# Kernel tuning notes

Hardware: AMD Instinct MI355X
Metric: run time of the kernel (lower is better)

The kernel has to match this reference:

```python
import jax, jax.numpy as jnp
import numpy as np

N = 2097152  # batch of 3x3 matrices


def setup_inputs() -> dict:
    key = jax.random.key(0)
    k1, k2 = jax.random.split(key)
    rotation = jax.random.normal(k1, (N, 3, 3), dtype=jnp.float32)
    # learned parameter: eye(3) + 1e-3 * randn, per __init__
    mat = jnp.eye(3, dtype=jnp.float32) + 0.001 * jax.random.normal(k2, (3, 3), dtype=jnp.float32)
    return {"rotation": rotation, "mat": mat}


def reference(rotation, mat):
    # new_mat = mat @ rotation (mat broadcast over batch)  -> [N,3,3]
    new_mat = jnp.einsum('ab,nbc->nac', mat, rotation)
    # polar rotation factor via batched 3x3 SVD: R = U @ V^T
    U, S, Vh = jnp.linalg.svd(new_mat, full_matrices=False)
    out = jnp.einsum('nab,nbc->nac', U, Vh)  # torch: U @ V.transpose == U @ Vh
    logdet = jnp.zeros((rotation.shape[0],), dtype=rotation.dtype)
    return out, logdet
```

## Files before the change

kernel.cpp:

```cpp
#include <hip/hip_runtime.h>
#include <math.h>


typedef float v2f __attribute__((ext_vector_type(2)));
typedef float v4f __attribute__((ext_vector_type(4)));

#define NEWTON_ITERS 6
#define NS_ITERS 2

__device__ __forceinline__ void polar_pair(
    v2f& x00, v2f& x01, v2f& x02,
    v2f& x10, v2f& x11, v2f& x12,
    v2f& x20, v2f& x21, v2f& x22)
{
    #pragma unroll
    for (int it = 0; it < NEWTON_ITERS; ++it) {
        v2f c00 = x11*x22 - x12*x21;
        v2f c01 = x12*x20 - x10*x22;
        v2f c02 = x10*x21 - x11*x20;
        v2f c10 = x02*x21 - x01*x22;
        v2f c11 = x00*x22 - x02*x20;
        v2f c12 = x01*x20 - x00*x21;
        v2f c20 = x01*x12 - x02*x11;
        v2f c21 = x02*x10 - x00*x12;
        v2f c22 = x00*x11 - x01*x10;

        v2f det = x00*c00 + x01*c01 + x02*c02;

        float d0 = det.x, d1 = det.y;
        float ad0 = fmaxf(fabsf(d0), 1e-30f);
        float ad1 = fmaxf(fabsf(d1), 1e-30f);
        float z0 = __builtin_amdgcn_exp2f(__builtin_amdgcn_logf(ad0) * (-1.0f/3.0f));
        float z1 = __builtin_amdgcn_exp2f(__builtin_amdgcn_logf(ad1) * (-1.0f/3.0f));
        v2f s = {0.5f * z0, 0.5f * z1};
        v2f u = {copysignf(0.5f * z0 * z0, d0), copysignf(0.5f * z1 * z1, d1)};

        x00 = s*x00 + u*c00;  x01 = s*x01 + u*c01;  x02 = s*x02 + u*c02;
        x10 = s*x10 + u*c10;  x11 = s*x11 + u*c11;  x12 = s*x12 + u*c12;
        x20 = s*x20 + u*c20;  x21 = s*x21 + u*c21;  x22 = s*x22 + u*c22;
    }

    #pragma unroll
    for (int it = 0; it < NS_ITERS; ++it) {
        v2f s00 = x00*x00 + x10*x10 + x20*x20;
        v2f s01 = x00*x01 + x10*x11 + x20*x21;
        v2f s02 = x00*x02 + x10*x12 + x20*x22;
        v2f s11 = x01*x01 + x11*x11 + x21*x21;
        v2f s12 = x01*x02 + x11*x12 + x21*x22;
        v2f s22 = x02*x02 + x12*x12 + x22*x22;
        v2f t00 = 1.5f - 0.5f*s00, t01 = -0.5f*s01, t02 = -0.5f*s02;
        v2f t11 = 1.5f - 0.5f*s11, t12 = -0.5f*s12;
        v2f t22 = 1.5f - 0.5f*s22;
        v2f y00 = x00*t00 + x01*t01 + x02*t02;
        v2f y01 = x00*t01 + x01*t11 + x02*t12;
        v2f y02 = x00*t02 + x01*t12 + x02*t22;
        v2f y10 = x10*t00 + x11*t01 + x12*t02;
        v2f y11 = x10*t01 + x11*t11 + x12*t12;
        v2f y12 = x10*t02 + x11*t12 + x12*t22;
        v2f y20 = x20*t00 + x21*t01 + x22*t02;
        v2f y21 = x20*t01 + x21*t11 + x22*t12;
        v2f y22 = x20*t02 + x21*t12 + x22*t22;
        x00=y00; x01=y01; x02=y02;
        x10=y10; x11=y11; x12=y12;
        x20=y20; x21=y21; x22=y22;
    }
}

__device__ __forceinline__ void compute_tile(
    float* buf, int lane, float* outBase,
    float m00, float m01, float m02,
    float m10, float m11, float m12,
    float m20, float m21, float m22)
{
    const float* L = buf + lane * 18;
    v2f r00 = {L[0], L[9]},  r01 = {L[1], L[10]}, r02 = {L[2], L[11]};
    v2f r10 = {L[3], L[12]}, r11 = {L[4], L[13]}, r12 = {L[5], L[14]};
    v2f r20 = {L[6], L[15]}, r21 = {L[7], L[16]}, r22 = {L[8], L[17]};

    v2f x00 = m00*r00 + m01*r10 + m02*r20;
    v2f x01 = m00*r01 + m01*r11 + m02*r21;
    v2f x02 = m00*r02 + m01*r12 + m02*r22;
    v2f x10 = m10*r00 + m11*r10 + m12*r20;
    v2f x11 = m10*r01 + m11*r11 + m12*r21;
    v2f x12 = m10*r02 + m11*r12 + m12*r22;
    v2f x20 = m20*r00 + m21*r10 + m22*r20;
    v2f x21 = m20*r01 + m21*r11 + m22*r21;
    v2f x22 = m20*r02 + m21*r12 + m22*r22;

    polar_pair(x00,x01,x02,x10,x11,x12,x20,x21,x22);

    float* S = buf + lane * 18;
    S[0]=x00.x; S[9] =x00.y; S[1]=x01.x; S[10]=x01.y; S[2]=x02.x; S[11]=x02.y;
    S[3]=x10.x; S[12]=x10.y; S[4]=x11.x; S[13]=x11.y; S[5]=x12.x; S[14]=x12.y;
    S[6]=x20.x; S[15]=x20.y; S[7]=x21.x; S[16]=x21.y; S[8]=x22.x; S[17]=x22.y;

    v4f* g4 = (v4f*)outBase;
    const v4f* l4 = (const v4f*)buf;
    #pragma unroll
    for (int k = 0; k < 4; ++k)
        g4[k * 64 + lane] = l4[k * 64 + lane];
    ((v2f*)(outBase + 1024))[lane] = ((const v2f*)(buf + 1024))[lane];
}

__device__ __forceinline__ void stage_tile(const float* gsrc, float* buf, int lane)
{
    #pragma unroll
    for (int k = 0; k < 4; ++k) {
        __builtin_amdgcn_global_load_lds(
            (const __attribute__((address_space(1))) void*)(gsrc + k * 256 + lane * 4),
            (__attribute__((address_space(3))) void*)(buf + k * 256),
            16, 0, 0);
    }
    #pragma unroll
    for (int k = 0; k < 2; ++k) {
        __builtin_amdgcn_global_load_lds(
            (const __attribute__((address_space(1))) void*)(gsrc + 1024 + k * 64 + lane),
            (__attribute__((address_space(3))) void*)(buf + 1024 + k * 64),
            4, 0, 0);
    }
}

__global__ __launch_bounds__(256) void polar3x3_pipe_kernel(
    const float* __restrict__ rot,
    const float* __restrict__ mat,
    float* __restrict__ out,
    int n)
{
    __shared__ __align__(16) float lds[9216];
    const int t    = threadIdx.x;
    const int lane = t & 63;
    const int w    = t >> 6;
    const long long blockBase = (long long)blockIdx.x * 1024;
    const long long waveBase  = blockBase + (long long)w * 256;
    float* buf0 = lds + w * 2304;
    float* buf1 = buf0 + 1152;

    const float m00 = mat[0], m01 = mat[1], m02 = mat[2];
    const float m10 = mat[3], m11 = mat[4], m12 = mat[5];
    const float m20 = mat[6], m21 = mat[7], m22 = mat[8];

    const bool full = (blockBase + 1024 <= (long long)n);

    if (full) {
        stage_tile(rot + waveBase * 9, buf0, lane);
        stage_tile(rot + (waveBase + 128) * 9, buf1, lane);

        asm volatile("s_waitcnt vmcnt(6)" ::: "memory");

        v4f* ld4 = (v4f*)(out + (long long)n * 9 + waveBase);
        __builtin_nontemporal_store(v4f{0.f, 0.f, 0.f, 0.f}, ld4 + lane);

        compute_tile(buf0, lane, out + waveBase * 9,
                     m00,m01,m02,m10,m11,m12,m20,m21,m22);

        asm volatile("s_waitcnt vmcnt(6)" ::: "memory");

        compute_tile(buf1, lane, out + (waveBase + 128) * 9,
                     m00,m01,m02,m10,m11,m12,m20,m21,m22);
    } else {
        #pragma unroll
        for (int tile = 0; tile < 2; ++tile) {
            long long tileBase = waveBase + tile * 128;
            v2f r00,r01,r02,r10,r11,r12,r20,r21,r22;
            #pragma unroll
            for (int q = 0; q < 2; ++q) {
                long long mi = tileBase + 2 * lane + q;
                if (mi < (long long)n) {
                    const float* r = rot + mi * 9;
                    r00[q]=r[0]; r01[q]=r[1]; r02[q]=r[2];
                    r10[q]=r[3]; r11[q]=r[4]; r12[q]=r[5];
                    r20[q]=r[6]; r21[q]=r[7]; r22[q]=r[8];
                } else {
                    r00[q]=1.f; r01[q]=0.f; r02[q]=0.f;
                    r10[q]=0.f; r11[q]=1.f; r12[q]=0.f;
                    r20[q]=0.f; r21[q]=0.f; r22[q]=1.f;
                }
            }
            v2f x00 = m00*r00 + m01*r10 + m02*r20;
            v2f x01 = m00*r01 + m01*r11 + m02*r21;
            v2f x02 = m00*r02 + m01*r12 + m02*r22;
            v2f x10 = m10*r00 + m11*r10 + m12*r20;
            v2f x11 = m10*r01 + m11*r11 + m12*r21;
            v2f x12 = m10*r02 + m11*r12 + m12*r22;
            v2f x20 = m20*r00 + m21*r10 + m22*r20;
            v2f x21 = m20*r01 + m21*r11 + m22*r21;
            v2f x22 = m20*r02 + m21*r12 + m22*r22;
            polar_pair(x00,x01,x02,x10,x11,x12,x20,x21,x22);
            #pragma unroll
            for (int q = 0; q < 2; ++q) {
                long long mi = tileBase + 2 * lane + q;
                if (mi < (long long)n) {
                    float* o = out + mi * 9;
                    o[0]=x00[q]; o[1]=x01[q]; o[2]=x02[q];
                    o[3]=x10[q]; o[4]=x11[q]; o[5]=x12[q];
                    o[6]=x20[q]; o[7]=x21[q]; o[8]=x22[q];
                    out[(long long)n * 9 + mi] = 0.0f;
                }
            }
        }
    }
}

extern "C" void kernel_launch(void* const* d_in, const int* in_sizes, int n_in,
                              void* d_out, int out_size, void* d_ws, size_t ws_size,
                              hipStream_t stream) {
    const float* rot = (const float*)d_in[0];
    const float* mat = (const float*)d_in[1];
    float* out = (float*)d_out;

    int n = in_sizes[0] / 9;
    int block = 256;
    int grid = (n + 1023) / 1024;
    polar3x3_pipe_kernel<<<grid, block, 0, stream>>>(rot, mat, out, n);
}
```

Measured before the change: 30.61 us.

## Double each wave's work with four-tile LDS ping-pong pipeline and nontemporal stores

Each wave now handles 512 matrices as four 128-matrix tiles instead of two. After a tile is computed and stored, the next tile is staged into the freed LDS buffer, so global loads overlap with compute and vmcnt waits are retuned to match. Output stores become nontemporal, and the logdet zero stores are issued up front. The grid halves, which lowers wave count and occupancy-based latency hiding, and the vmcnt counts must exactly match the outstanding store and load ordering.

```diff
diff --git a/kernel.cpp b/kernel.cpp
--- a/kernel.cpp
+++ b/kernel.cpp
@@ -66,7 +66,25 @@
     }
 }
 
-__device__ __forceinline__ void compute_tile(
+__device__ __forceinline__ void stage_tile(const float* gsrc, float* buf, int lane)
+{
+    #pragma unroll
+    for (int k = 0; k < 4; ++k) {
+        __builtin_amdgcn_global_load_lds(
+            (const __attribute__((address_space(1))) void*)(gsrc + k * 256 + lane * 4),
+            (__attribute__((address_space(3))) void*)(buf + k * 256),
+            16, 0, 0);
+    }
+    #pragma unroll
+    for (int k = 0; k < 2; ++k) {
+        __builtin_amdgcn_global_load_lds(
+            (const __attribute__((address_space(1))) void*)(gsrc + 1024 + k * 64 + lane),
+            (__attribute__((address_space(3))) void*)(buf + 1024 + k * 64),
+            4, 0, 0);
+    }
+}
+
+__device__ __forceinline__ void compute_store_tile(
     float* buf, int lane, float* outBase,
     float m00, float m01, float m02,
     float m10, float m11, float m12,
@@ -98,29 +116,12 @@
     const v4f* l4 = (const v4f*)buf;
     #pragma unroll
     for (int k = 0; k < 4; ++k)
-        g4[k * 64 + lane] = l4[k * 64 + lane];
-    ((v2f*)(outBase + 1024))[lane] = ((const v2f*)(buf + 1024))[lane];
-}
-
-__device__ __forceinline__ void stage_tile(const float* gsrc, float* buf, int lane)
-{
-    #pragma unroll
-    for (int k = 0; k < 4; ++k) {
-        __builtin_amdgcn_global_load_lds(
-            (const __attribute__((address_space(1))) void*)(gsrc + k * 256 + lane * 4),
-            (__attribute__((address_space(3))) void*)(buf + k * 256),
-            16, 0, 0);
-    }
-    #pragma unroll
-    for (int k = 0; k < 2; ++k) {
-        __builtin_amdgcn_global_load_lds(
-            (const __attribute__((address_space(1))) void*)(gsrc + 1024 + k * 64 + lane),
-            (__attribute__((address_space(3))) void*)(buf + 1024 + k * 64),
-            4, 0, 0);
-    }
-}
-
-__global__ __launch_bounds__(256) void polar3x3_pipe_kernel(
+        __builtin_nontemporal_store(l4[k * 64 + lane], g4 + k * 64 + lane);
+    __builtin_nontemporal_store(((const v2f*)(buf + 1024))[lane],
+                                (v2f*)(outBase + 1024) + lane);
+}
+
+__global__ __launch_bounds__(256) void polar3x3_ss_kernel(
     const float* __restrict__ rot,
     const float* __restrict__ mat,
     float* __restrict__ out,
@@ -130,8 +131,8 @@
     const int t    = threadIdx.x;
     const int lane = t & 63;
     const int w    = t >> 6;
-    const long long blockBase = (long long)blockIdx.x * 1024;
-    const long long waveBase  = blockBase + (long long)w * 256;
+    const long long blockBase = (long long)blockIdx.x * 2048;
+    const long long waveBase  = blockBase + (long long)w * 512;
     float* buf0 = lds + w * 2304;
     float* buf1 = buf0 + 1152;
 
@@ -139,28 +140,37 @@
     const float m10 = mat[3], m11 = mat[4], m12 = mat[5];
     const float m20 = mat[6], m21 = mat[7], m22 = mat[8];
 
-    const bool full = (blockBase + 1024 <= (long long)n);
+    const bool full = (blockBase + 2048 <= (long long)n);
 
     if (full) {
-        stage_tile(rot + waveBase * 9, buf0, lane);
-        stage_tile(rot + (waveBase + 128) * 9, buf1, lane);
+        v4f* ld4 = (v4f*)(out + (long long)n * 9 + waveBase);
+        __builtin_nontemporal_store(v4f{0.f,0.f,0.f,0.f}, ld4 + lane);
+        __builtin_nontemporal_store(v4f{0.f,0.f,0.f,0.f}, ld4 + 64 + lane);
+
+        stage_tile(rot + waveBase * 9,           buf0, lane);
+        stage_tile(rot + (waveBase + 128) * 9,   buf1, lane);
 
         asm volatile("s_waitcnt vmcnt(6)" ::: "memory");
-
-        v4f* ld4 = (v4f*)(out + (long long)n * 9 + waveBase);
-        __builtin_nontemporal_store(v4f{0.f, 0.f, 0.f, 0.f}, ld4 + lane);
-
-        compute_tile(buf0, lane, out + waveBase * 9,
-                     m00,m01,m02,m10,m11,m12,m20,m21,m22);
-
-        asm volatile("s_waitcnt vmcnt(6)" ::: "memory");
-
-        compute_tile(buf1, lane, out + (waveBase + 128) * 9,
-                     m00,m01,m02,m10,m11,m12,m20,m21,m22);
+        compute_store_tile(buf0, lane, out + waveBase * 9,
+                           m00,m01,m02,m10,m11,m12,m20,m21,m22);
+        stage_tile(rot + (waveBase + 256) * 9, buf0, lane);
+
+        asm volatile("s_waitcnt vmcnt(11)" ::: "memory");
+        compute_store_tile(buf1, lane, out + (waveBase + 128) * 9,
+                           m00,m01,m02,m10,m11,m12,m20,m21,m22);
+        stage_tile(rot + (waveBase + 384) * 9, buf1, lane);
+
+        asm volatile("s_waitcnt vmcnt(11)" ::: "memory");
+        compute_store_tile(buf0, lane, out + (waveBase + 256) * 9,
+                           m00,m01,m02,m10,m11,m12,m20,m21,m22);
+
+        asm volatile("s_waitcnt vmcnt(5)" ::: "memory");
+        compute_store_tile(buf1, lane, out + (waveBase + 384) * 9,
+                           m00,m01,m02,m10,m11,m12,m20,m21,m22);
     } else {
-        #pragma unroll
-        for (int tile = 0; tile < 2; ++tile) {
-            long long tileBase = waveBase + tile * 128;
+        #pragma unroll 1
+        for (int tile = 0; tile < 4; ++tile) {
+            long long tileBase = waveBase + (long long)tile * 128;
             v2f r00,r01,r02,r10,r11,r12,r20,r21,r22;
             #pragma unroll
             for (int q = 0; q < 2; ++q) {
@@ -210,6 +220,6 @@
 
     int n = in_sizes[0] / 9;
     int block = 256;
-    int grid = (n + 1023) / 1024;
-    polar3x3_pipe_kernel<<<grid, block, 0, stream>>>(rot, mat, out, n);
-}
+    int grid = (n + 2047) / 2048;
+    polar3x3_ss_kernel<<<grid, block, 0, stream>>>(rot, mat, out, n);
+}
```

After: 31.23 us. +2.0%, slower.
